# Kernel optimization log

Measured on AMD Instinct MI355X. Metric: run time of the kernel, lower is better.

Reference implementation:

```python
import jax, jax.numpy as jnp
import numpy as np

B, S, V = 2, 336, 8      # batch, seq_len, n_vars
D, H, P = 256, 8, 96     # d_model, num_heads, pred_len
DK = D // H
OUT_CHN = 8
EPS = 1e-5


def _layernorm(x, g, b):
    mu = jnp.mean(x, axis=-1, keepdims=True)
    var = jnp.var(x, axis=-1, keepdims=True)
    return (x - mu) * jax.lax.rsqrt(var + EPS) * g + b


def _attn_ff(src, Wq, bq, Wk, bk, Wv, bv, Wo, bo, ln1_g, ln1_b):
    # src: [N, L, D]; manual MHA + residual + layernorm (dropout=0)
    N, L, _ = src.shape
    q = (src @ Wq + bq).reshape(N, L, H, DK).transpose(0, 2, 1, 3)
    k = (src @ Wk + bk).reshape(N, L, H, DK).transpose(0, 2, 1, 3)
    v = (src @ Wv + bv).reshape(N, L, H, DK).transpose(0, 2, 1, 3)
    scores = jnp.einsum('nhqd,nhkd->nhqk', q, k) / np.sqrt(DK).astype(np.float32)
    attn = jax.nn.softmax(scores, axis=-1)
    o = jnp.einsum('nhqk,nhkd->nhqd', attn, v)
    o = o.transpose(0, 2, 1, 3).reshape(N, L, D) @ Wo + bo
    return _layernorm(src + o, ln1_g, ln1_b)


def setup_inputs() -> dict:
    key = jax.random.key(0)
    ks = jax.random.split(key, 8)
    s = 1.0 / np.sqrt(D)
    return {
        'x': jax.random.normal(ks[0], (B, S, V), dtype=jnp.float32),
        'emb_w': jax.random.normal(ks[1], (1, D), dtype=jnp.float32),
        'emb_b': jnp.zeros((D,), jnp.float32),
        'Wq': jax.random.normal(ks[2], (D, D), dtype=jnp.float32) * s,
        'bq': jnp.zeros((D,), jnp.float32),
        'Wk': jax.random.normal(ks[3], (D, D), dtype=jnp.float32) * s,
        'bk': jnp.zeros((D,), jnp.float32),
        'Wv': jax.random.normal(ks[4], (D, D), dtype=jnp.float32) * s,
        'bv': jnp.zeros((D,), jnp.float32),
        'Wo': jax.random.normal(ks[5], (D, D), dtype=jnp.float32) * s,
        'bo': jnp.zeros((D,), jnp.float32),
        'ln1_g': jnp.ones((D,), jnp.float32),
        'ln1_b': jnp.zeros((D,), jnp.float32),
        'norm_g': jnp.ones((D,), jnp.float32),
        'norm_b': jnp.zeros((D,), jnp.float32),
        'proj_w': jax.random.normal(ks[6], (S * D, P), dtype=jnp.float32) / np.sqrt(S * D).astype(np.float32),
        'proj_b': jnp.zeros((P,), jnp.float32),
    }


def reference(x, emb_w, emb_b, Wq, bq, Wk, bk, Wv, bv, Wo, bo,
              ln1_g, ln1_b, norm_g, norm_b, proj_w, proj_b):
    attn_p = (Wq, bq, Wk, bk, Wv, bv, Wo, bo, ln1_g, ln1_b)
    # x: [B,S,V] -> [B,V,S] -> embed each scalar to D
    e = x.transpose(0, 2, 1)[..., None] @ emb_w + emb_b  # [B,V,S,D]
    for _ in range(10):
        # attention over time axis (shared weights)
        e = _attn_ff(e.reshape(B * V, S, D), *attn_p).reshape(B, V, S, D)
        e = _layernorm(e.transpose(0, 2, 1, 3), norm_g, norm_b)  # [B,S,V,D]
        # attention over variable axis (same weights)
        e = _attn_ff(e.reshape(B * S, V, D), *attn_p).reshape(B, S, V, D)
        e = e.transpose(0, 2, 1, 3)  # [B,V,S,D]
    out = e.reshape(B, V, S * D) @ proj_w + proj_b  # [B,V,P]
    return out.transpose(0, 2, 1)[:, :, :OUT_CHN]  # [B,P,out_chn]
```

## Files before the change

kernel.cpp:

```cpp
#include <hip/hip_runtime.h>

#define SS 336
#define VV 8
#define DD 256
#define DKK 32
#define NTOK 5376
#define NTD (NTOK * DD)
#define ATT_SCALE 0.17677669529663687f
#define LN_EPS 1e-5f

typedef _Float16 f16x8 __attribute__((ext_vector_type(8)));
typedef _Float16 f16x4v __attribute__((ext_vector_type(4)));
typedef __attribute__((ext_vector_type(4))) float f32x4;

__device__ inline _Float16 f2h(float f) { return (_Float16)f; }

__global__ __launch_bounds__(256) void k_prep_w(
    const float* __restrict__ Wq, const float* __restrict__ Wk,
    const float* __restrict__ Wv, const float* __restrict__ Wo,
    _Float16* __restrict__ WT2) {
  int z = blockIdx.y;
  const float* W = (z == 0) ? Wq : (z == 1) ? Wk : (z == 2) ? Wv : Wo;
  int o = blockIdx.x * 256 + threadIdx.x;
  int blk = o >> 9;
// ... 64 lines not shown
    }
  }

  float bsv[4];
#pragma unroll
  for (int nt = 0; nt < 4; ++nt) bsv[nt] = bias[(ntb + nt) * 16 + lcol];
#pragma unroll
  for (int mt = 0; mt < 2; ++mt) {
#pragma unroll
    for (int i = 0; i < 4; ++i) {
      int r = m0 + wm * 32 + mt * 16 + quad * 4 + i;
#pragma unroll
      for (int nt = 0; nt < 4; ++nt) {
        int c = (ntb + nt) * 16 + lcol;
        H[(size_t)r * 256 + c] = f2h(acc[mt][nt][i] + bsv[nt]);
      }
    }
  }
}

#define KSTR 36
#define VTSTR 344
#define PSTR 72
__global__ __launch_bounds__(512) void k_attn_time(
    const _Float16* __restrict__ Q, const _Float16* __restrict__ K,
    const _Float16* __restrict__ V, _Float16* __restrict__ O16) {
  int qg = blockIdx.x, h = blockIdx.y, n = blockIdx.z;
  int tid = threadIdx.x;
  int wave = tid >> 6, lane = tid & 63;
  int quad = lane >> 4, lcol = lane & 15;

  __shared__ _Float16 Ks[336 * KSTR];
  __shared__ _Float16 Vt[32 * VTSTR + 16];
  __shared__ _Float16 Ps[8][16 * PSTR];

  const size_t base = (size_t)(n * SS) * DD + h * DKK;

  for (int c = tid; c < 1344; c += 512) {
    int row = c >> 2, part = c & 3;
    f16x8 kv = *(const f16x8*)&K[base + (size_t)row * DD + part * 8];
    f16x4v klo = __builtin_shufflevector(kv, kv, 0, 1, 2, 3);
    f16x4v khi = __builtin_shufflevector(kv, kv, 4, 5, 6, 7);
    *(f16x4v*)&Ks[row * KSTR + part * 8] = klo;
    *(f16x4v*)&Ks[row * KSTR + part * 8 + 4] = khi;
    f16x8 vv = *(const f16x8*)&V[base + (size_t)row * DD + part * 8];
#pragma unroll
    for (int j = 0; j < 8; ++j) Vt[(part * 8 + j) * VTSTR + row] = vv[j];
  }
  for (int c = tid; c < 272; c += 512) {
    if (c < 256) {
      int d = c >> 3, col = 336 + (c & 7);
      Vt[d * VTSTR + col] = (_Float16)0.f;
    } else {
      Vt[32 * VTSTR + (c - 256)] = (_Float16)0.f;
    }
  }
  __syncthreads();

  _Float16* P = Ps[wave];
  const f16x8 onesv = {(_Float16)1.f, (_Float16)1.f, (_Float16)1.f, (_Float16)1.f,
                       (_Float16)1.f, (_Float16)1.f, (_Float16)1.f, (_Float16)1.f};
  const f32x4 z4 = {0.f, 0.f, 0.f, 0.f};

  int qt0 = qg ? 11 : 0;
  int qtend = qg ? 21 : 11;
  for (int qtile = qt0 + wave; qtile < qtend; qtile += 8) {
    int qb = qtile * 16;

    f16x8 qf = *(const f16x8*)&Q[base + (size_t)(qb + lcol) * DD + quad * 8];
    f32x4 accA = {0.f, 0.f, 0.f, 0.f};
    f32x4 accB = {0.f, 0.f, 0.f, 0.f};
    f32x4 lacc = {0.f, 0.f, 0.f, 0.f};
    float m_[4] = {-1e30f, -1e30f, -1e30f, -1e30f};

    for (int T = 0; T < 6; ++T) {
      int k0 = T * 64;
      bool full = (T < 5);
      f32x4 s[4];
      {
        const _Float16* kp = &Ks[(k0 + lcol) * KSTR + quad * 8];
        f16x4v a0 = *(const f16x4v*)kp;
        f16x4v b0 = *(const f16x4v*)(kp + 4);
        f16x8 kf = __builtin_shufflevector(a0, b0, 0, 1, 2, 3, 4, 5, 6, 7);
        s[0] = __builtin_amdgcn_mfma_f32_16x16x32_f16(qf, kf, z4, 0, 0, 0);
      }
      if (full) {
#pragma unroll
        for (int u = 1; u < 4; ++u) {
          const _Float16* kp = &Ks[(k0 + u * 16 + lcol) * KSTR + quad * 8];
          f16x4v a0 = *(const f16x4v*)kp;
          f16x4v b0 = *(const f16x4v*)(kp + 4);
          f16x8 kf = __builtin_shufflevector(a0, b0, 0, 1, 2, 3, 4, 5, 6, 7);
          s[u] = __builtin_amdgcn_mfma_f32_16x16x32_f16(qf, kf, z4, 0, 0, 0);
        }
      } else {
        s[1] = z4; s[2] = z4; s[3] = z4;
      }
      float sc[4][4], p[4][4], corr[4];
#pragma unroll
      for (int u = 0; u < 4; ++u)
#pragma unroll
        for (int i = 0; i < 4; ++i)
          sc[u][i] = (u == 0 || full) ? s[u][i] * ATT_SCALE : -1e30f;
#pragma unroll
      for (int i = 0; i < 4; ++i) {
        float t2 = fmaxf(fmaxf(sc[0][i], sc[1][i]), fmaxf(sc[2][i], sc[3][i]));
        t2 = fmaxf(t2, __shfl_xor(t2, 1));
        t2 = fmaxf(t2, __shfl_xor(t2, 2));
        t2 = fmaxf(t2, __shfl_xor(t2, 4));
        t2 = fmaxf(t2, __shfl_xor(t2, 8));
        float nm = fmaxf(m_[i], t2);
        corr[i] = __expf(m_[i] - nm);
        m_[i] = nm;
#pragma unroll
        for (int u = 0; u < 4; ++u) p[u][i] = __expf(sc[u][i] - nm);
        accA[i] *= corr[i];
        accB[i] *= corr[i];
        lacc[i] *= corr[i];
      }
#pragma unroll
      for (int i = 0; i < 4; ++i)
#pragma unroll
        for (int u = 0; u < 4; ++u)
          P[(quad * 4 + i) * PSTR + u * 16 + lcol] = f2h(p[u][i]);
      f16x8 pf0 = *(const f16x8*)&P[lcol * PSTR + quad * 8];
      lacc = __builtin_amdgcn_mfma_f32_16x16x32_f16(pf0, onesv, lacc, 0, 0, 0);
      f16x8 va0 = *(const f16x8*)&Vt[lcol * VTSTR + k0 + quad * 8];
      f16x8 vb0 = *(const f16x8*)&Vt[(16 + lcol) * VTSTR + k0 + quad * 8];
      accA = __builtin_amdgcn_mfma_f32_16x16x32_f16(pf0, va0, accA, 0, 0, 0);
      accB = __builtin_amdgcn_mfma_f32_16x16x32_f16(pf0, vb0, accB, 0, 0, 0);
      if (full) {
        f16x8 pf1 = *(const f16x8*)&P[lcol * PSTR + 32 + quad * 8];
        lacc = __builtin_amdgcn_mfma_f32_16x16x32_f16(pf1, onesv, lacc, 0, 0, 0);
        f16x8 va1 = *(const f16x8*)&Vt[lcol * VTSTR + k0 + 32 + quad * 8];
        f16x8 vb1 = *(const f16x8*)&Vt[(16 + lcol) * VTSTR + k0 + 32 + quad * 8];
        accA = __builtin_amdgcn_mfma_f32_16x16x32_f16(pf1, va1, accA, 0, 0, 0);
        accB = __builtin_amdgcn_mfma_f32_16x16x32_f16(pf1, vb1, accB, 0, 0, 0);
      }
    }

#pragma unroll
    for (int i = 0; i < 4; ++i) {
      float inv = 1.f / lacc[i];
      P[(quad * 4 + i) * PSTR + lcol] = f2h(accA[i] * inv);
      P[(quad * 4 + i) * PSTR + 16 + lcol] = f2h(accB[i] * inv);
    }
    int row = lane >> 2, seg = lane & 3;
    f16x8 ov = *(const f16x8*)&P[row * PSTR + seg * 8];
    *(f16x8*)&O16[base + (size_t)(qb + row) * DD + seg * 8] = ov;
  }
}

__global__ __launch_bounds__(512) void k_mega_var(
    const _Float16* __restrict__ AO16, const _Float16* __restrict__ WT2,
    const float* __restrict__ bq, const float* __restrict__ bk,
    const float* __restrict__ bv, const float* __restrict__ bo,
    const float* __restrict__ g1, const float* __restrict__ c1,
    const float* __restrict__ gn, const float* __restrict__ bn,
    float* __restrict__ Etime, _Float16* __restrict__ Q16,
    _Float16* __restrict__ K16, _Float16* __restrict__ V16, int doqkv) {
  int tid = threadIdx.x;
  int wave = tid >> 6, lane = tid & 63;
  int quad = lane >> 4, lcol = lane & 15;

  __shared__ int rmapS[32];
  __shared__ _Float16 Af[32 * 264];
  __shared__ float Cf[32 * 260];
  __shared__ _Float16 QKVs[32 * 776];

  if (tid < 32) {
    int r2 = blockIdx.x * 32 + tid;
    int n_idx = r2 >> 3, v = r2 & 7;
    int b = n_idx / SS, s = n_idx - b * SS;
    rmapS[tid] = (b * VV + v) * SS + s;
  }
  __syncthreads();

  {
    int row = tid >> 4, seg = tid & 15;
    const _Float16* src = AO16 + (size_t)rmapS[row] * DD + seg * 16;
    _Float16* dst = Af + row * 264 + seg * 16;
    *(f16x8*)(dst) = *(const f16x8*)(src);
    *(f16x8*)(dst + 8) = *(const f16x8*)(src + 8);
  }
  __syncthreads();

  const _Float16* WoF = WT2 + (size_t)3 * 65536;

  {
    f32x4 acc[2][2] = {};
    for (int kb = 0; kb < 8; ++kb) {
      int k0 = kb * 32;
      f16x8 af0 = *(const f16x8*)&Af[lcol * 264 + k0 + quad * 8];
      f16x8 af1 = *(const f16x8*)&Af[(16 + lcol) * 264 + k0 + quad * 8];
#pragma unroll
      for (int nt = 0; nt < 2; ++nt) {
        f16x8 bfr = *(const f16x8*)&WoF[((wave * 2 + nt) * 8 + kb) * 512 + lane * 8];
        acc[0][nt] = __builtin_amdgcn_mfma_f32_16x16x32_f16(af0, bfr, acc[0][nt], 0, 0, 0);
        acc[1][nt] = __builtin_amdgcn_mfma_f32_16x16x32_f16(af1, bfr, acc[1][nt], 0, 0, 0);
      }
    }
#pragma unroll
    for (int mt = 0; mt < 2; ++mt) {
#pragma unroll
      for (int i = 0; i < 4; ++i) {
        int row = mt * 16 + quad * 4 + i;
        size_t rb = (size_t)rmapS[row] * 256;
#pragma unroll
        for (int nt = 0; nt < 2; ++nt) {
          int col = (wave * 2 + nt) * 16 + lcol;
          Cf[row * 260 + col] = acc[mt][nt][i] + bo[col] + Etime[rb + col];
        }
      }
    }
  }
  __syncthreads();

  {
    int row = tid >> 4, c0 = (tid & 15) * 16;
    float v[16];
#pragma unroll
    for (int j = 0; j < 16; ++j) v[j] = Cf[row * 260 + c0 + j];
#pragma unroll
    for (int pass = 0; pass < 2; ++pass) {
      const float* gg = pass ? gn : g1;
      const float* bb = pass ? bn : c1;
      float s = 0.f, q = 0.f;
#pragma unroll
      for (int j = 0; j < 16; ++j) { s += v[j]; q = fmaf(v[j], v[j], q); }
      s += __shfl_xor(s, 1); q += __shfl_xor(q, 1);
      s += __shfl_xor(s, 2); q += __shfl_xor(q, 2);
      s += __shfl_xor(s, 4); q += __shfl_xor(q, 4);
      s += __shfl_xor(s, 8); q += __shfl_xor(q, 8);
      float mu = s * (1.0f / 256.0f);
      float rs = rsqrtf(q * (1.0f / 256.0f) - mu * mu + LN_EPS);
#pragma unroll
      for (int j = 0; j < 16; ++j)
        v[j] = fmaf((v[j] - mu) * rs, gg[c0 + j], bb[c0 + j]);
    }
#pragma unroll
    for (int j = 0; j < 16; ++j) Cf[row * 260 + c0 + j] = v[j];
#pragma unroll
    for (int j8 = 0; j8 < 2; ++j8) {
      f16x8 h;
#pragma unroll
      for (int jj = 0; jj < 8; ++jj) h[jj] = f2h(v[j8 * 8 + jj]);
      *(f16x8*)&Af[row * 264 + c0 + j8 * 8] = h;
    }
  }
  __syncthreads();

  {
    f32x4 acc[2][6] = {};
    for (int kb = 0; kb < 8; ++kb) {
      int k0 = kb * 32;
      f16x8 af0 = *(const f16x8*)&Af[lcol * 264 + k0 + quad * 8];
      f16x8 af1 = *(const f16x8*)&Af[(16 + lcol) * 264 + k0 + quad * 8];
#pragma unroll
      for (int j = 0; j < 6; ++j) {
        int ntg = wave * 6 + j;
        f16x8 bfr = *(const f16x8*)&WT2[(size_t)(ntg * 8 + kb) * 512 + lane * 8];
        acc[0][j] = __builtin_amdgcn_mfma_f32_16x16x32_f16(af0, bfr, acc[0][j], 0, 0, 0);
        acc[1][j] = __builtin_amdgcn_mfma_f32_16x16x32_f16(af1, bfr, acc[1][j], 0, 0, 0);
      }
    }
#pragma unroll
    for (int j = 0; j < 6; ++j) {
      int ntg = wave * 6 + j;
      int colb = ntg * 16;
      int z = colb >> 8, coln = (colb & 255) + lcol;
      const float* bz = (z == 0) ? bq : (z == 1) ? bk : bv;
      float bval = bz[coln];
#pragma unroll
      for (int mt = 0; mt < 2; ++mt) {
#pragma unroll
        for (int i = 0; i < 4; ++i)
          QKVs[(mt * 16 + quad * 4 + i) * 776 + colb + lcol] = f2h(acc[mt][j][i] + bval);
      }
    }
  }
  __syncthreads();

  {
    int half = tid & 1, qi = (tid >> 1) & 7, h = (tid >> 4) & 7, ng = tid >> 7;
    int d0 = h * 32 + half * 16;
    const _Float16* Qp = &QKVs[(ng * 8 + qi) * 776 + d0];
    float qv[16];
#pragma unroll
    for (int j8 = 0; j8 < 2; ++j8) {
      f16x8 t = *(const f16x8*)(Qp + j8 * 8);
#pragma unroll
      for (int jj = 0; jj < 8; ++jj) qv[j8 * 8 + jj] = (float)t[jj];
    }
    float sc[8];
#pragma unroll
    for (int k = 0; k < 8; ++k) {
      const _Float16* Kp = &QKVs[(ng * 8 + k) * 776 + 256 + d0];
      float s = 0.f;
#pragma unroll
      for (int j8 = 0; j8 < 2; ++j8) {
        f16x8 t = *(const f16x8*)(Kp + j8 * 8);
#pragma unroll
        for (int jj = 0; jj < 8; ++jj) s = fmaf(qv[j8 * 8 + jj], (float)t[jj], s);
      }
      sc[k] = s;
    }
#pragma unroll
    for (int k = 0; k < 8; ++k)
      sc[k] = (sc[k] + __shfl_xor(sc[k], 1)) * ATT_SCALE;
    float mx = sc[0];
#pragma unroll
    for (int k = 1; k < 8; ++k) mx = fmaxf(mx, sc[k]);
    float ps = 0.f;
#pragma unroll
    for (int k = 0; k < 8; ++k) { sc[k] = __expf(sc[k] - mx); ps += sc[k]; }
    float inv = 1.f / ps;
    float ov[16];
#pragma unroll
    for (int j = 0; j < 16; ++j) ov[j] = 0.f;
#pragma unroll
    for (int k = 0; k < 8; ++k) {
      const _Float16* Vp = &QKVs[(ng * 8 + k) * 776 + 512 + d0];
      float p = sc[k];
#pragma unroll
      for (int j8 = 0; j8 < 2; ++j8) {
        f16x8 t = *(const f16x8*)(Vp + j8 * 8);
#pragma unroll
        for (int jj = 0; jj < 8; ++jj)
          ov[j8 * 8 + jj] = fmaf(p, (float)t[jj], ov[j8 * 8 + jj]);
      }
    }
    _Float16* Op = &Af[(ng * 8 + qi) * 264 + d0];
#pragma unroll
    for (int j8 = 0; j8 < 2; ++j8) {
      f16x8 hh;
#pragma unroll
      for (int jj = 0; jj < 8; ++jj) hh[jj] = f2h(ov[j8 * 8 + jj] * inv);
      *(f16x8*)(Op + j8 * 8) = hh;
    }
  }
  __syncthreads();

  {
    f32x4 acc[2][2] = {};
    for (int kb = 0; kb < 8; ++kb) {
      int k0 = kb * 32;
      f16x8 af0 = *(const f16x8*)&Af[lcol * 264 + k0 + quad * 8];
      f16x8 af1 = *(const f16x8*)&Af[(16 + lcol) * 264 + k0 + quad * 8];
#pragma unroll
      for (int nt = 0; nt < 2; ++nt) {
        f16x8 bfr = *(const f16x8*)&WoF[((wave * 2 + nt) * 8 + kb) * 512 + lane * 8];
        acc[0][nt] = __builtin_amdgcn_mfma_f32_16x16x32_f16(af0, bfr, acc[0][nt], 0, 0, 0);
        acc[1][nt] = __builtin_amdgcn_mfma_f32_16x16x32_f16(af1, bfr, acc[1][nt], 0, 0, 0);
      }
    }
#pragma unroll
    for (int mt = 0; mt < 2; ++mt) {
#pragma unroll
      for (int i = 0; i < 4; ++i) {
        int row = mt * 16 + quad * 4 + i;
#pragma unroll
        for (int nt = 0; nt < 2; ++nt) {
          int col = (wave * 2 + nt) * 16 + lcol;
          Cf[row * 260 + col] = acc[mt][nt][i] + bo[col] + Cf[row * 260 + col];
        }
      }
    }
  }
  __syncthreads();

  {
    int row = tid >> 4, c0 = (tid & 15) * 16;
    float v[16];
#pragma unroll
    for (int j = 0; j < 16; ++j) v[j] = Cf[row * 260 + c0 + j];
    float s = 0.f, q = 0.f;
#pragma unroll
    for (int j = 0; j < 16; ++j) { s += v[j]; q = fmaf(v[j], v[j], q); }
    s += __shfl_xor(s, 1); q += __shfl_xor(q, 1);
    s += __shfl_xor(s, 2); q += __shfl_xor(q, 2);
    s += __shfl_xor(s, 4); q += __shfl_xor(q, 4);
    s += __shfl_xor(s, 8); q += __shfl_xor(q, 8);
    float mu = s * (1.0f / 256.0f);
    float rs = rsqrtf(q * (1.0f / 256.0f) - mu * mu + LN_EPS);
#pragma unroll
    for (int j = 0; j < 16; ++j)
      v[j] = fmaf((v[j] - mu) * rs, g1[c0 + j], c1[c0 + j]);
    size_t rb = (size_t)rmapS[row] * 256 + c0;
#pragma unroll
    for (int j4 = 0; j4 < 4; ++j4) {
      float4 f4 = make_float4(v[j4 * 4], v[j4 * 4 + 1], v[j4 * 4 + 2], v[j4 * 4 + 3]);
      *(float4*)&Etime[rb + j4 * 4] = f4;
    }
#pragma unroll
    for (int j8 = 0; j8 < 2; ++j8) {
      f16x8 hh;
#pragma unroll
      for (int jj = 0; jj < 8; ++jj) hh[jj] = f2h(v[j8 * 8 + jj]);
      *(f16x8*)&Af[row * 264 + c0 + j8 * 8] = hh;
    }
  }
  __syncthreads();

  if (doqkv) {
    f32x4 acc[2][6] = {};
    for (int kb = 0; kb < 8; ++kb) {
      int k0 = kb * 32;
      f16x8 af0 = *(const f16x8*)&Af[lcol * 264 + k0 + quad * 8];
      f16x8 af1 = *(const f16x8*)&Af[(16 + lcol) * 264 + k0 + quad * 8];
#pragma unroll
      for (int j = 0; j < 6; ++j) {
        int ntg = wave * 6 + j;
        f16x8 bfr = *(const f16x8*)&WT2[(size_t)(ntg * 8 + kb) * 512 + lane * 8];
        acc[0][j] = __builtin_amdgcn_mfma_f32_16x16x32_f16(af0, bfr, acc[0][j], 0, 0, 0);
        acc[1][j] = __builtin_amdgcn_mfma_f32_16x16x32_f16(af1, bfr, acc[1][j], 0, 0, 0);
      }
    }
#pragma unroll
    for (int j = 0; j < 6; ++j) {
      int ntg = wave * 6 + j;
      int colb = ntg * 16;
      int z = colb >> 8, coln = (colb & 255) + lcol;
      const float* bz = (z == 0) ? bq : (z == 1) ? bk : bv;
      _Float16* Hd = (z == 0) ? Q16 : (z == 1) ? K16 : V16;
      float bval = bz[coln];
#pragma unroll
      for (int mt = 0; mt < 2; ++mt) {
#pragma unroll
        for (int i = 0; i < 4; ++i) {
          int row = mt * 16 + quad * 4 + i;
          Hd[(size_t)rmapS[row] * 256 + coln] = f2h(acc[mt][j][i] + bval);
        }
      }
    }
  }
}

__global__ __launch_bounds__(192) void k_proj_partial(
    const float* __restrict__ E, const float* __restrict__ PW,
    float* __restrict__ Part) {
  int kc = blockIdx.x;
  int tid = threadIdx.x;
  int p4 = tid % 24, g = tid / 24;
  __shared__ float Es[16][128];
  __shared__ float sm[8][1536];
  for (int idx = tid; idx < 512; idx += 192) {
    int row = idx >> 5, kk4 = idx & 31;
    *(float4*)&Es[row][kk4 * 4] =
        *(const float4*)&E[(size_t)row * 86016 + kc * 128 + kk4 * 4];
  }
  __syncthreads();
  float4 acc[16];
#pragma unroll
  for (int i = 0; i < 16; ++i) acc[i] = make_float4(0.f, 0.f, 0.f, 0.f);
  for (int j = 0; j < 16; ++j) {
    int k = g * 16 + j;
    float4 w = *(const float4*)&PW[(size_t)(kc * 128 + k) * 96 + p4 * 4];
// ... 61 lines not shown
  const float* bo = (const float*)d_in[10];
  const float* g1 = (const float*)d_in[11];
  const float* b1 = (const float*)d_in[12];
  const float* gn = (const float*)d_in[13];
  const float* bn = (const float*)d_in[14];
  const float* PW = (const float*)d_in[15];
  const float* PB = (const float*)d_in[16];
  float* out = (float*)d_out;

  float* ws = (float*)d_ws;
  float* Etime   = ws;
  _Float16* Et16 = (_Float16*)(ws + (size_t)NTD);
  _Float16* Q16  = (_Float16*)(ws + (size_t)NTD + NTD / 2);
  _Float16* K16  = Q16 + (size_t)NTD;
  _Float16* V16  = K16 + (size_t)NTD;
  _Float16* AO16 = V16 + (size_t)NTD;
  _Float16* WT2  = AO16 + (size_t)NTD;
  float* Part    = (float*)(WT2 + 4 * 65536);

  k_prep_w<<<dim3(256, 4), 256, 0, stream>>>(Wq, Wk, Wv, Wo, WT2);
  k_embed<<<NTOK, 256, 0, stream>>>(x, emb_w, emb_b, Etime, Et16);
  k_gemm_qkv<<<dim3(84, 2, 3), 256, 0, stream>>>(
      Et16, WT2, bq, bk, bv, Q16, K16, V16);
  for (int it = 0; it < 10; ++it) {
    k_attn_time<<<dim3(2, 8, 16), 512, 0, stream>>>(Q16, K16, V16, AO16);
    k_mega_var<<<168, 512, 0, stream>>>(
        AO16, WT2, bq, bk, bv, bo, g1, b1, gn, bn, Etime,
        Q16, K16, V16, (it < 9) ? 1 : 0);
  }
  k_proj_partial<<<672, 192, 0, stream>>>(Etime, PW, Part);
  k_proj_reduce<<<96, 256, 0, stream>>>(Part, PB, out);
}
```

Baseline: 571.8 us.

## Fuse 10-iteration attention loop into one persistent cooperative kernel with grid syncs

Replaces the 20 per-iteration launches of the time-attention and variable-attention kernels with a single cooperative kernel of 256 blocks. Inside it, the two phases are separated by grid.sync and share one raw shared-memory buffer. This removes kernel launch and drain gaps between stages. In exchange it adds grid-wide barriers, and in the variable phase only 168 of the 256 blocks do work. It also requires all 256 blocks, each using about 100KB of shared memory, to be co-resident.

```diff
diff --git a/kernel.cpp b/kernel.cpp
--- a/kernel.cpp
+++ b/kernel.cpp
@@ -1,4 +1,7 @@
 #include <hip/hip_runtime.h>
+#include <hip/hip_cooperative_groups.h>
+
+namespace cg = cooperative_groups;
 
 #define SS 336
 #define VV 8
@@ -110,417 +113,425 @@
 #define KSTR 36
 #define VTSTR 344
 #define PSTR 72
-__global__ __launch_bounds__(512) void k_attn_time(
-    const _Float16* __restrict__ Q, const _Float16* __restrict__ K,
-    const _Float16* __restrict__ V, _Float16* __restrict__ O16) {
-  int qg = blockIdx.x, h = blockIdx.y, n = blockIdx.z;
-  int tid = threadIdx.x;
-  int wave = tid >> 6, lane = tid & 63;
-  int quad = lane >> 4, lcol = lane & 15;
-
-  __shared__ _Float16 Ks[336 * KSTR];
-  __shared__ _Float16 Vt[32 * VTSTR + 16];
-  __shared__ _Float16 Ps[8][16 * PSTR];
-
-  const size_t base = (size_t)(n * SS) * DD + h * DKK;
-
-  for (int c = tid; c < 1344; c += 512) {
-    int row = c >> 2, part = c & 3;
-    f16x8 kv = *(const f16x8*)&K[base + (size_t)row * DD + part * 8];
-    f16x4v klo = __builtin_shufflevector(kv, kv, 0, 1, 2, 3);
-    f16x4v khi = __builtin_shufflevector(kv, kv, 4, 5, 6, 7);
-    *(f16x4v*)&Ks[row * KSTR + part * 8] = klo;
-    *(f16x4v*)&Ks[row * KSTR + part * 8 + 4] = khi;
-    f16x8 vv = *(const f16x8*)&V[base + (size_t)row * DD + part * 8];
-#pragma unroll
-    for (int j = 0; j < 8; ++j) Vt[(part * 8 + j) * VTSTR + row] = vv[j];
-  }
-  for (int c = tid; c < 272; c += 512) {
-    if (c < 256) {
-      int d = c >> 3, col = 336 + (c & 7);
-      Vt[d * VTSTR + col] = (_Float16)0.f;
-    } else {
-      Vt[32 * VTSTR + (c - 256)] = (_Float16)0.f;
-    }
-  }
-  __syncthreads();
-
-  _Float16* P = Ps[wave];
-  const f16x8 onesv = {(_Float16)1.f, (_Float16)1.f, (_Float16)1.f, (_Float16)1.f,
-                       (_Float16)1.f, (_Float16)1.f, (_Float16)1.f, (_Float16)1.f};
-  const f32x4 z4 = {0.f, 0.f, 0.f, 0.f};
-
-  int qt0 = qg ? 11 : 0;
-  int qtend = qg ? 21 : 11;
-  for (int qtile = qt0 + wave; qtile < qtend; qtile += 8) {
-    int qb = qtile * 16;
-
-    f16x8 qf = *(const f16x8*)&Q[base + (size_t)(qb + lcol) * DD + quad * 8];
-    f32x4 accA = {0.f, 0.f, 0.f, 0.f};
-    f32x4 accB = {0.f, 0.f, 0.f, 0.f};
-    f32x4 lacc = {0.f, 0.f, 0.f, 0.f};
-    float m_[4] = {-1e30f, -1e30f, -1e30f, -1e30f};
-
-    for (int T = 0; T < 6; ++T) {
-      int k0 = T * 64;
-      bool full = (T < 5);
-      f32x4 s[4];
-      {
-        const _Float16* kp = &Ks[(k0 + lcol) * KSTR + quad * 8];
-        f16x4v a0 = *(const f16x4v*)kp;
-        f16x4v b0 = *(const f16x4v*)(kp + 4);
-        f16x8 kf = __builtin_shufflevector(a0, b0, 0, 1, 2, 3, 4, 5, 6, 7);
-        s[0] = __builtin_amdgcn_mfma_f32_16x16x32_f16(qf, kf, z4, 0, 0, 0);
-      }
-      if (full) {
-#pragma unroll
-        for (int u = 1; u < 4; ++u) {
-          const _Float16* kp = &Ks[(k0 + u * 16 + lcol) * KSTR + quad * 8];
-          f16x4v a0 = *(const f16x4v*)kp;
-          f16x4v b0 = *(const f16x4v*)(kp + 4);
-          f16x8 kf = __builtin_shufflevector(a0, b0, 0, 1, 2, 3, 4, 5, 6, 7);
-          s[u] = __builtin_amdgcn_mfma_f32_16x16x32_f16(qf, kf, z4, 0, 0, 0);
-        }
-      } else {
-        s[1] = z4; s[2] = z4; s[3] = z4;
-      }
-      float sc[4][4], p[4][4], corr[4];
-#pragma unroll
-      for (int u = 0; u < 4; ++u)
-#pragma unroll
-        for (int i = 0; i < 4; ++i)
-          sc[u][i] = (u == 0 || full) ? s[u][i] * ATT_SCALE : -1e30f;
-#pragma unroll
-      for (int i = 0; i < 4; ++i) {
-        float t2 = fmaxf(fmaxf(sc[0][i], sc[1][i]), fmaxf(sc[2][i], sc[3][i]));
-        t2 = fmaxf(t2, __shfl_xor(t2, 1));
-        t2 = fmaxf(t2, __shfl_xor(t2, 2));
-        t2 = fmaxf(t2, __shfl_xor(t2, 4));
-        t2 = fmaxf(t2, __shfl_xor(t2, 8));
-        float nm = fmaxf(m_[i], t2);
-        corr[i] = __expf(m_[i] - nm);
-        m_[i] = nm;
-#pragma unroll
-        for (int u = 0; u < 4; ++u) p[u][i] = __expf(sc[u][i] - nm);
-        accA[i] *= corr[i];
-        accB[i] *= corr[i];
-        lacc[i] *= corr[i];
-      }
-#pragma unroll
-      for (int i = 0; i < 4; ++i)
-#pragma unroll
-        for (int u = 0; u < 4; ++u)
-          P[(quad * 4 + i) * PSTR + u * 16 + lcol] = f2h(p[u][i]);
-      f16x8 pf0 = *(const f16x8*)&P[lcol * PSTR + quad * 8];
-      lacc = __builtin_amdgcn_mfma_f32_16x16x32_f16(pf0, onesv, lacc, 0, 0, 0);
-      f16x8 va0 = *(const f16x8*)&Vt[lcol * VTSTR + k0 + quad * 8];
-      f16x8 vb0 = *(const f16x8*)&Vt[(16 + lcol) * VTSTR + k0 + quad * 8];
-      accA = __builtin_amdgcn_mfma_f32_16x16x32_f16(pf0, va0, accA, 0, 0, 0);
-      accB = __builtin_amdgcn_mfma_f32_16x16x32_f16(pf0, vb0, accB, 0, 0, 0);
-      if (full) {
-        f16x8 pf1 = *(const f16x8*)&P[lcol * PSTR + 32 + quad * 8];
-        lacc = __builtin_amdgcn_mfma_f32_16x16x32_f16(pf1, onesv, lacc, 0, 0, 0);
-        f16x8 va1 = *(const f16x8*)&Vt[lcol * VTSTR + k0 + 32 + quad * 8];
-        f16x8 vb1 = *(const f16x8*)&Vt[(16 + lcol) * VTSTR + k0 + 32 + quad * 8];
-        accA = __builtin_amdgcn_mfma_f32_16x16x32_f16(pf1, va1, accA, 0, 0, 0);
-        accB = __builtin_amdgcn_mfma_f32_16x16x32_f16(pf1, vb1, accB, 0, 0, 0);
-      }
-    }
-
-#pragma unroll
-    for (int i = 0; i < 4; ++i) {
-      float inv = 1.f / lacc[i];
-      P[(quad * 4 + i) * PSTR + lcol] = f2h(accA[i] * inv);
-      P[(quad * 4 + i) * PSTR + 16 + lcol] = f2h(accB[i] * inv);
-    }
-    int row = lane >> 2, seg = lane & 3;
-    f16x8 ov = *(const f16x8*)&P[row * PSTR + seg * 8];
-    *(f16x8*)&O16[base + (size_t)(qb + row) * DD + seg * 8] = ov;
-  }
-}
-
-__global__ __launch_bounds__(512) void k_mega_var(
-    const _Float16* __restrict__ AO16, const _Float16* __restrict__ WT2,
+
+__global__ __launch_bounds__(512) void k_loop(
+    _Float16* __restrict__ Q16, _Float16* __restrict__ K16,
+    _Float16* __restrict__ V16, _Float16* __restrict__ AO16,
+    const _Float16* __restrict__ WT2,
     const float* __restrict__ bq, const float* __restrict__ bk,
     const float* __restrict__ bv, const float* __restrict__ bo,
     const float* __restrict__ g1, const float* __restrict__ c1,
     const float* __restrict__ gn, const float* __restrict__ bn,
-    float* __restrict__ Etime, _Float16* __restrict__ Q16,
-    _Float16* __restrict__ K16, _Float16* __restrict__ V16, int doqkv) {
+    float* __restrict__ Etime) {
+  cg::grid_group grid = cg::this_grid();
+
+  __shared__ __align__(16) char SMRAW[99968];
+
+  int bid = blockIdx.x;
   int tid = threadIdx.x;
   int wave = tid >> 6, lane = tid & 63;
   int quad = lane >> 4, lcol = lane & 15;
 
-  __shared__ int rmapS[32];
-  __shared__ _Float16 Af[32 * 264];
-  __shared__ float Cf[32 * 260];
-  __shared__ _Float16 QKVs[32 * 776];
-
-  if (tid < 32) {
-    int r2 = blockIdx.x * 32 + tid;
-    int n_idx = r2 >> 3, v = r2 & 7;
-    int b = n_idx / SS, s = n_idx - b * SS;
-    rmapS[tid] = (b * VV + v) * SS + s;
-  }
-  __syncthreads();
-
-  {
-    int row = tid >> 4, seg = tid & 15;
-    const _Float16* src = AO16 + (size_t)rmapS[row] * DD + seg * 16;
-    _Float16* dst = Af + row * 264 + seg * 16;
-    *(f16x8*)(dst) = *(const f16x8*)(src);
-    *(f16x8*)(dst + 8) = *(const f16x8*)(src + 8);
-  }
-  __syncthreads();
-
   const _Float16* WoF = WT2 + (size_t)3 * 65536;
 
-  {
-    f32x4 acc[2][2] = {};
-    for (int kb = 0; kb < 8; ++kb) {
-      int k0 = kb * 32;
-      f16x8 af0 = *(const f16x8*)&Af[lcol * 264 + k0 + quad * 8];
-      f16x8 af1 = *(const f16x8*)&Af[(16 + lcol) * 264 + k0 + quad * 8];
-#pragma unroll
-      for (int nt = 0; nt < 2; ++nt) {
-        f16x8 bfr = *(const f16x8*)&WoF[((wave * 2 + nt) * 8 + kb) * 512 + lane * 8];
-        acc[0][nt] = __builtin_amdgcn_mfma_f32_16x16x32_f16(af0, bfr, acc[0][nt], 0, 0, 0);
-        acc[1][nt] = __builtin_amdgcn_mfma_f32_16x16x32_f16(af1, bfr, acc[1][nt], 0, 0, 0);
+  for (int it = 0; it < 10; ++it) {
+    {
+      _Float16* Ks  = (_Float16*)SMRAW;
+      _Float16* Vt  = (_Float16*)(SMRAW + 24192);
+      _Float16* PsB = (_Float16*)(SMRAW + 46240);
+
+      int qg = bid & 1, h = (bid >> 1) & 7, n = bid >> 4;
+      const size_t base = (size_t)(n * SS) * DD + h * DKK;
+
+      for (int c = tid; c < 1344; c += 512) {
+        int row = c >> 2, part = c & 3;
+        f16x8 kv = *(const f16x8*)&K16[base + (size_t)row * DD + part * 8];
+        f16x4v klo = __builtin_shufflevector(kv, kv, 0, 1, 2, 3);
+        f16x4v khi = __builtin_shufflevector(kv, kv, 4, 5, 6, 7);
+        *(f16x4v*)&Ks[row * KSTR + part * 8] = klo;
+        *(f16x4v*)&Ks[row * KSTR + part * 8 + 4] = khi;
+        f16x8 vv = *(const f16x8*)&V16[base + (size_t)row * DD + part * 8];
+#pragma unroll
+        for (int j = 0; j < 8; ++j) Vt[(part * 8 + j) * VTSTR + row] = vv[j];
+      }
+      for (int c = tid; c < 272; c += 512) {
+        if (c < 256) {
+          int d = c >> 3, col = 336 + (c & 7);
+          Vt[d * VTSTR + col] = (_Float16)0.f;
+        } else {
+          Vt[32 * VTSTR + (c - 256)] = (_Float16)0.f;
+        }
+      }
+      __syncthreads();
+
+      _Float16* P = PsB + wave * (16 * PSTR);
+      const f16x8 onesv = {(_Float16)1.f, (_Float16)1.f, (_Float16)1.f, (_Float16)1.f,
+                           (_Float16)1.f, (_Float16)1.f, (_Float16)1.f, (_Float16)1.f};
+      const f32x4 z4 = {0.f, 0.f, 0.f, 0.f};
+
+      int qt0 = qg ? 11 : 0;
+      int qtend = qg ? 21 : 11;
+      for (int qtile = qt0 + wave; qtile < qtend; qtile += 8) {
+        int qb = qtile * 16;
+
+        f16x8 qf = *(const f16x8*)&Q16[base + (size_t)(qb + lcol) * DD + quad * 8];
+        f32x4 accA = {0.f, 0.f, 0.f, 0.f};
+        f32x4 accB = {0.f, 0.f, 0.f, 0.f};
+        f32x4 lacc = {0.f, 0.f, 0.f, 0.f};
+        float m_[4] = {-1e30f, -1e30f, -1e30f, -1e30f};
+
+        for (int T = 0; T < 6; ++T) {
+          int k0 = T * 64;
+          bool full = (T < 5);
+          f32x4 s[4];
+          {
+            const _Float16* kp = &Ks[(k0 + lcol) * KSTR + quad * 8];
+            f16x4v a0 = *(const f16x4v*)kp;
+            f16x4v b0 = *(const f16x4v*)(kp + 4);
+            f16x8 kf = __builtin_shufflevector(a0, b0, 0, 1, 2, 3, 4, 5, 6, 7);
+            s[0] = __builtin_amdgcn_mfma_f32_16x16x32_f16(qf, kf, z4, 0, 0, 0);
+          }
+          if (full) {
+#pragma unroll
+            for (int u = 1; u < 4; ++u) {
+              const _Float16* kp = &Ks[(k0 + u * 16 + lcol) * KSTR + quad * 8];
+              f16x4v a0 = *(const f16x4v*)kp;
+              f16x4v b0 = *(const f16x4v*)(kp + 4);
+              f16x8 kf = __builtin_shufflevector(a0, b0, 0, 1, 2, 3, 4, 5, 6, 7);
+              s[u] = __builtin_amdgcn_mfma_f32_16x16x32_f16(qf, kf, z4, 0, 0, 0);
+            }
+          } else {
+            s[1] = z4; s[2] = z4; s[3] = z4;
+          }
+          float sc[4][4], p[4][4], corr[4];
+#pragma unroll
+          for (int u = 0; u < 4; ++u)
+#pragma unroll
+            for (int i = 0; i < 4; ++i)
+              sc[u][i] = (u == 0 || full) ? s[u][i] * ATT_SCALE : -1e30f;
+#pragma unroll
+          for (int i = 0; i < 4; ++i) {
+            float t2 = fmaxf(fmaxf(sc[0][i], sc[1][i]), fmaxf(sc[2][i], sc[3][i]));
+            t2 = fmaxf(t2, __shfl_xor(t2, 1));
+            t2 = fmaxf(t2, __shfl_xor(t2, 2));
+            t2 = fmaxf(t2, __shfl_xor(t2, 4));
+            t2 = fmaxf(t2, __shfl_xor(t2, 8));
+            float nm = fmaxf(m_[i], t2);
+            corr[i] = __expf(m_[i] - nm);
+            m_[i] = nm;
+#pragma unroll
+            for (int u = 0; u < 4; ++u) p[u][i] = __expf(sc[u][i] - nm);
+            accA[i] *= corr[i];
+            accB[i] *= corr[i];
+            lacc[i] *= corr[i];
+          }
+#pragma unroll
+          for (int i = 0; i < 4; ++i)
+#pragma unroll
+            for (int u = 0; u < 4; ++u)
+              P[(quad * 4 + i) * PSTR + u * 16 + lcol] = f2h(p[u][i]);
+          f16x8 pf0 = *(const f16x8*)&P[lcol * PSTR + quad * 8];
+          lacc = __builtin_amdgcn_mfma_f32_16x16x32_f16(pf0, onesv, lacc, 0, 0, 0);
+          f16x8 va0 = *(const f16x8*)&Vt[lcol * VTSTR + k0 + quad * 8];
+          f16x8 vb0 = *(const f16x8*)&Vt[(16 + lcol) * VTSTR + k0 + quad * 8];
+          accA = __builtin_amdgcn_mfma_f32_16x16x32_f16(pf0, va0, accA, 0, 0, 0);
+          accB = __builtin_amdgcn_mfma_f32_16x16x32_f16(pf0, vb0, accB, 0, 0, 0);
+          if (full) {
+            f16x8 pf1 = *(const f16x8*)&P[lcol * PSTR + 32 + quad * 8];
+            lacc = __builtin_amdgcn_mfma_f32_16x16x32_f16(pf1, onesv, lacc, 0, 0, 0);
+            f16x8 va1 = *(const f16x8*)&Vt[lcol * VTSTR + k0 + 32 + quad * 8];
+            f16x8 vb1 = *(const f16x8*)&Vt[(16 + lcol) * VTSTR + k0 + 32 + quad * 8];
+            accA = __builtin_amdgcn_mfma_f32_16x16x32_f16(pf1, va1, accA, 0, 0, 0);
+            accB = __builtin_amdgcn_mfma_f32_16x16x32_f16(pf1, vb1, accB, 0, 0, 0);
+          }
+        }
+
+#pragma unroll
+        for (int i = 0; i < 4; ++i) {
+          float inv = 1.f / lacc[i];
+          P[(quad * 4 + i) * PSTR + lcol] = f2h(accA[i] * inv);
+          P[(quad * 4 + i) * PSTR + 16 + lcol] = f2h(accB[i] * inv);
+        }
+        int row = lane >> 2, seg = lane & 3;
+        f16x8 ov = *(const f16x8*)&P[row * PSTR + seg * 8];
+        *(f16x8*)&AO16[base + (size_t)(qb + row) * DD + seg * 8] = ov;
       }
     }
-#pragma unroll
-    for (int mt = 0; mt < 2; ++mt) {
-#pragma unroll
-      for (int i = 0; i < 4; ++i) {
-        int row = mt * 16 + quad * 4 + i;
-        size_t rb = (size_t)rmapS[row] * 256;
-#pragma unroll
-        for (int nt = 0; nt < 2; ++nt) {
-          int col = (wave * 2 + nt) * 16 + lcol;
-          Cf[row * 260 + col] = acc[mt][nt][i] + bo[col] + Etime[rb + col];
+    grid.sync();
+
+    if (bid < 168) {
+      int* rmapS     = (int*)SMRAW;
+      _Float16* Af   = (_Float16*)(SMRAW + 128);
+      float* Cf      = (float*)(SMRAW + 17024);
+      _Float16* QKVs = (_Float16*)(SMRAW + 50304);
+      int doqkv = (it < 9) ? 1 : 0;
+
+      if (tid < 32) {
+        int r2 = bid * 32 + tid;
+        int n_idx = r2 >> 3, v = r2 & 7;
+        int b = n_idx / SS, s = n_idx - b * SS;
+        rmapS[tid] = (b * VV + v) * SS + s;
+      }
+      __syncthreads();
+
+      {
+        int row = tid >> 4, seg = tid & 15;
+        const _Float16* src = AO16 + (size_t)rmapS[row] * DD + seg * 16;
+        _Float16* dst = Af + row * 264 + seg * 16;
+        *(f16x8*)(dst) = *(const f16x8*)(src);
+        *(f16x8*)(dst + 8) = *(const f16x8*)(src + 8);
+      }
+      __syncthreads();
+
+      {
+        f32x4 acc[2][2] = {};
+        for (int kb = 0; kb < 8; ++kb) {
+          int k0 = kb * 32;
+          f16x8 af0 = *(const f16x8*)&Af[lcol * 264 + k0 + quad * 8];
+          f16x8 af1 = *(const f16x8*)&Af[(16 + lcol) * 264 + k0 + quad * 8];
+#pragma unroll
+          for (int nt = 0; nt < 2; ++nt) {
+            f16x8 bfr = *(const f16x8*)&WoF[((wave * 2 + nt) * 8 + kb) * 512 + lane * 8];
+            acc[0][nt] = __builtin_amdgcn_mfma_f32_16x16x32_f16(af0, bfr, acc[0][nt], 0, 0, 0);
+            acc[1][nt] = __builtin_amdgcn_mfma_f32_16x16x32_f16(af1, bfr, acc[1][nt], 0, 0, 0);
+          }
+        }
+#pragma unroll
+        for (int mt = 0; mt < 2; ++mt) {
+#pragma unroll
+          for (int i = 0; i < 4; ++i) {
+            int row = mt * 16 + quad * 4 + i;
+            size_t rb = (size_t)rmapS[row] * 256;
+#pragma unroll
+            for (int nt = 0; nt < 2; ++nt) {
+              int col = (wave * 2 + nt) * 16 + lcol;
+              Cf[row * 260 + col] = acc[mt][nt][i] + bo[col] + Etime[rb + col];
+            }
+          }
+        }
+      }
+      __syncthreads();
+
+      {
+        int row = tid >> 4, c0 = (tid & 15) * 16;
+        float v[16];
+#pragma unroll
+        for (int j = 0; j < 16; ++j) v[j] = Cf[row * 260 + c0 + j];
+#pragma unroll
+        for (int pass = 0; pass < 2; ++pass) {
+          const float* gg = pass ? gn : g1;
+          const float* bb = pass ? bn : c1;
+          float s = 0.f, q = 0.f;
+#pragma unroll
+          for (int j = 0; j < 16; ++j) { s += v[j]; q = fmaf(v[j], v[j], q); }
+          s += __shfl_xor(s, 1); q += __shfl_xor(q, 1);
+          s += __shfl_xor(s, 2); q += __shfl_xor(q, 2);
+          s += __shfl_xor(s, 4); q += __shfl_xor(q, 4);
+          s += __shfl_xor(s, 8); q += __shfl_xor(q, 8);
+          float mu = s * (1.0f / 256.0f);
+          float rs = rsqrtf(q * (1.0f / 256.0f) - mu * mu + LN_EPS);
+#pragma unroll
+          for (int j = 0; j < 16; ++j)
+            v[j] = fmaf((v[j] - mu) * rs, gg[c0 + j], bb[c0 + j]);
+        }
+#pragma unroll
+        for (int j = 0; j < 16; ++j) Cf[row * 260 + c0 + j] = v[j];
+#pragma unroll
+        for (int j8 = 0; j8 < 2; ++j8) {
+          f16x8 h;
+#pragma unroll
+          for (int jj = 0; jj < 8; ++jj) h[jj] = f2h(v[j8 * 8 + jj]);
+          *(f16x8*)&Af[row * 264 + c0 + j8 * 8] = h;
+        }
+      }
+      __syncthreads();
+
+      {
+        f32x4 acc[2][6] = {};
+        for (int kb = 0; kb < 8; ++kb) {
+          int k0 = kb * 32;
+          f16x8 af0 = *(const f16x8*)&Af[lcol * 264 + k0 + quad * 8];
+          f16x8 af1 = *(const f16x8*)&Af[(16 + lcol) * 264 + k0 + quad * 8];
+#pragma unroll
+          for (int j = 0; j < 6; ++j) {
+            int ntg = wave * 6 + j;
+            f16x8 bfr = *(const f16x8*)&WT2[(size_t)(ntg * 8 + kb) * 512 + lane * 8];
+            acc[0][j] = __builtin_amdgcn_mfma_f32_16x16x32_f16(af0, bfr, acc[0][j], 0, 0, 0);
+            acc[1][j] = __builtin_amdgcn_mfma_f32_16x16x32_f16(af1, bfr, acc[1][j], 0, 0, 0);
+          }
+        }
+#pragma unroll
+        for (int j = 0; j < 6; ++j) {
+          int ntg = wave * 6 + j;
+          int colb = ntg * 16;
+          int z = colb >> 8, coln = (colb & 255) + lcol;
+          const float* bz = (z == 0) ? bq : (z == 1) ? bk : bv;
+          float bval = bz[coln];
+#pragma unroll
+          for (int mt = 0; mt < 2; ++mt) {
+#pragma unroll
+            for (int i = 0; i < 4; ++i)
+              QKVs[(mt * 16 + quad * 4 + i) * 776 + colb + lcol] = f2h(acc[mt][j][i] + bval);
+          }
+        }
+      }
+      __syncthreads();
+
+      {
+        int half = tid & 1, qi = (tid >> 1) & 7, h = (tid >> 4) & 7, ng = tid >> 7;
+        int d0 = h * 32 + half * 16;
+        const _Float16* Qp = &QKVs[(ng * 8 + qi) * 776 + d0];
+        float qv[16];
+#pragma unroll
+        for (int j8 = 0; j8 < 2; ++j8) {
+          f16x8 t = *(const f16x8*)(Qp + j8 * 8);
+#pragma unroll
+          for (int jj = 0; jj < 8; ++jj) qv[j8 * 8 + jj] = (float)t[jj];
+        }
+        float sc[8];
+#pragma unroll
+        for (int k = 0; k < 8; ++k) {
+          const _Float16* Kp = &QKVs[(ng * 8 + k) * 776 + 256 + d0];
+          float s = 0.f;
+#pragma unroll
+          for (int j8 = 0; j8 < 2; ++j8) {
+            f16x8 t = *(const f16x8*)(Kp + j8 * 8);
+#pragma unroll
+            for (int jj = 0; jj < 8; ++jj) s = fmaf(qv[j8 * 8 + jj], (float)t[jj], s);
+          }
+          sc[k] = s;
+        }
+#pragma unroll
+        for (int k = 0; k < 8; ++k)
+          sc[k] = (sc[k] + __shfl_xor(sc[k], 1)) * ATT_SCALE;
+        float mx = sc[0];
+#pragma unroll
+        for (int k = 1; k < 8; ++k) mx = fmaxf(mx, sc[k]);
+        float ps = 0.f;
+#pragma unroll
+        for (int k = 0; k < 8; ++k) { sc[k] = __expf(sc[k] - mx); ps += sc[k]; }
+        float inv = 1.f / ps;
+        float ov[16];
+#pragma unroll
+        for (int j = 0; j < 16; ++j) ov[j] = 0.f;
+#pragma unroll
+        for (int k = 0; k < 8; ++k) {
+          const _Float16* Vp = &QKVs[(ng * 8 + k) * 776 + 512 + d0];
+          float p = sc[k];
+#pragma unroll
+          for (int j8 = 0; j8 < 2; ++j8) {
+            f16x8 t = *(const f16x8*)(Vp + j8 * 8);
+#pragma unroll
+            for (int jj = 0; jj < 8; ++jj)
+              ov[j8 * 8 + jj] = fmaf(p, (float)t[jj], ov[j8 * 8 + jj]);
+          }
+        }
+        _Float16* Op = &Af[(ng * 8 + qi) * 264 + d0];
+#pragma unroll
+        for (int j8 = 0; j8 < 2; ++j8) {
+          f16x8 hh;
+#pragma unroll
+          for (int jj = 0; jj < 8; ++jj) hh[jj] = f2h(ov[j8 * 8 + jj] * inv);
+          *(f16x8*)(Op + j8 * 8) = hh;
+        }
+      }
+      __syncthreads();
+
+      {
+        f32x4 acc[2][2] = {};
+        for (int kb = 0; kb < 8; ++kb) {
+          int k0 = kb * 32;
+          f16x8 af0 = *(const f16x8*)&Af[lcol * 264 + k0 + quad * 8];
+          f16x8 af1 = *(const f16x8*)&Af[(16 + lcol) * 264 + k0 + quad * 8];
+#pragma unroll
+          for (int nt = 0; nt < 2; ++nt) {
+            f16x8 bfr = *(const f16x8*)&WoF[((wave * 2 + nt) * 8 + kb) * 512 + lane * 8];
+            acc[0][nt] = __builtin_amdgcn_mfma_f32_16x16x32_f16(af0, bfr, acc[0][nt], 0, 0, 0);
+            acc[1][nt] = __builtin_amdgcn_mfma_f32_16x16x32_f16(af1, bfr, acc[1][nt], 0, 0, 0);
+          }
+        }
+#pragma unroll
+        for (int mt = 0; mt < 2; ++mt) {
+#pragma unroll
+          for (int i = 0; i < 4; ++i) {
+            int row = mt * 16 + quad * 4 + i;
+#pragma unroll
+            for (int nt = 0; nt < 2; ++nt) {
+              int col = (wave * 2 + nt) * 16 + lcol;
+              Cf[row * 260 + col] = acc[mt][nt][i] + bo[col] + Cf[row * 260 + col];
+            }
+          }
+        }
+      }
+      __syncthreads();
+
+      {
+        int row = tid >> 4, c0 = (tid & 15) * 16;
+        float v[16];
+#pragma unroll
+        for (int j = 0; j < 16; ++j) v[j] = Cf[row * 260 + c0 + j];
+        float s = 0.f, q = 0.f;
+#pragma unroll
+        for (int j = 0; j < 16; ++j) { s += v[j]; q = fmaf(v[j], v[j], q); }
+        s += __shfl_xor(s, 1); q += __shfl_xor(q, 1);
+        s += __shfl_xor(s, 2); q += __shfl_xor(q, 2);
+        s += __shfl_xor(s, 4); q += __shfl_xor(q, 4);
+        s += __shfl_xor(s, 8); q += __shfl_xor(q, 8);
+        float mu = s * (1.0f / 256.0f);
+        float rs = rsqrtf(q * (1.0f / 256.0f) - mu * mu + LN_EPS);
+#pragma unroll
+        for (int j = 0; j < 16; ++j)
+          v[j] = fmaf((v[j] - mu) * rs, g1[c0 + j], c1[c0 + j]);
+        size_t rb = (size_t)rmapS[row] * 256 + c0;
+#pragma unroll
+        for (int j4 = 0; j4 < 4; ++j4) {
+          float4 f4 = make_float4(v[j4 * 4], v[j4 * 4 + 1], v[j4 * 4 + 2], v[j4 * 4 + 3]);
+          *(float4*)&Etime[rb + j4 * 4] = f4;
+        }
+#pragma unroll
+        for (int j8 = 0; j8 < 2; ++j8) {
+          f16x8 hh;
+#pragma unroll
+          for (int jj = 0; jj < 8; ++jj) hh[jj] = f2h(v[j8 * 8 + jj]);
+          *(f16x8*)&Af[row * 264 + c0 + j8 * 8] = hh;
+        }
+      }
+      __syncthreads();
+
+      if (doqkv) {
+        f32x4 acc[2][6] = {};
+        for (int kb = 0; kb < 8; ++kb) {
+          int k0 = kb * 32;
+          f16x8 af0 = *(const f16x8*)&Af[lcol * 264 + k0 + quad * 8];
+          f16x8 af1 = *(const f16x8*)&Af[(16 + lcol) * 264 + k0 + quad * 8];
+#pragma unroll
+          for (int j = 0; j < 6; ++j) {
+            int ntg = wave * 6 + j;
+            f16x8 bfr = *(const f16x8*)&WT2[(size_t)(ntg * 8 + kb) * 512 + lane * 8];
+            acc[0][j] = __builtin_amdgcn_mfma_f32_16x16x32_f16(af0, bfr, acc[0][j], 0, 0, 0);
+            acc[1][j] = __builtin_amdgcn_mfma_f32_16x16x32_f16(af1, bfr, acc[1][j], 0, 0, 0);
+          }
+        }
+#pragma unroll
+        for (int j = 0; j < 6; ++j) {
+          int ntg = wave * 6 + j;
+          int colb = ntg * 16;
+          int z = colb >> 8, coln = (colb & 255) + lcol;
+          const float* bz = (z == 0) ? bq : (z == 1) ? bk : bv;
+          _Float16* Hd = (z == 0) ? Q16 : (z == 1) ? K16 : V16;
+          float bval = bz[coln];
+#pragma unroll
+          for (int mt = 0; mt < 2; ++mt) {
+#pragma unroll
+            for (int i = 0; i < 4; ++i) {
+              int row = mt * 16 + quad * 4 + i;
+              Hd[(size_t)rmapS[row] * 256 + coln] = f2h(acc[mt][j][i] + bval);
+            }
+          }
         }
       }
     }
-  }
-  __syncthreads();
-
-  {
-    int row = tid >> 4, c0 = (tid & 15) * 16;
-    float v[16];
-#pragma unroll
-    for (int j = 0; j < 16; ++j) v[j] = Cf[row * 260 + c0 + j];
-#pragma unroll
-    for (int pass = 0; pass < 2; ++pass) {
-      const float* gg = pass ? gn : g1;
-      const float* bb = pass ? bn : c1;
-      float s = 0.f, q = 0.f;
-#pragma unroll
-      for (int j = 0; j < 16; ++j) { s += v[j]; q = fmaf(v[j], v[j], q); }
-      s += __shfl_xor(s, 1); q += __shfl_xor(q, 1);
-      s += __shfl_xor(s, 2); q += __shfl_xor(q, 2);
-      s += __shfl_xor(s, 4); q += __shfl_xor(q, 4);
-      s += __shfl_xor(s, 8); q += __shfl_xor(q, 8);
-      float mu = s * (1.0f / 256.0f);
-      float rs = rsqrtf(q * (1.0f / 256.0f) - mu * mu + LN_EPS);
-#pragma unroll
-      for (int j = 0; j < 16; ++j)
-        v[j] = fmaf((v[j] - mu) * rs, gg[c0 + j], bb[c0 + j]);
-    }
-#pragma unroll
-    for (int j = 0; j < 16; ++j) Cf[row * 260 + c0 + j] = v[j];
-#pragma unroll
-    for (int j8 = 0; j8 < 2; ++j8) {
-      f16x8 h;
-#pragma unroll
-      for (int jj = 0; jj < 8; ++jj) h[jj] = f2h(v[j8 * 8 + jj]);
-      *(f16x8*)&Af[row * 264 + c0 + j8 * 8] = h;
-    }
-  }
-  __syncthreads();
-
-  {
-    f32x4 acc[2][6] = {};
-    for (int kb = 0; kb < 8; ++kb) {
-      int k0 = kb * 32;
-      f16x8 af0 = *(const f16x8*)&Af[lcol * 264 + k0 + quad * 8];
-      f16x8 af1 = *(const f16x8*)&Af[(16 + lcol) * 264 + k0 + quad * 8];
-#pragma unroll
-      for (int j = 0; j < 6; ++j) {
-        int ntg = wave * 6 + j;
-        f16x8 bfr = *(const f16x8*)&WT2[(size_t)(ntg * 8 + kb) * 512 + lane * 8];
-        acc[0][j] = __builtin_amdgcn_mfma_f32_16x16x32_f16(af0, bfr, acc[0][j], 0, 0, 0);
-        acc[1][j] = __builtin_amdgcn_mfma_f32_16x16x32_f16(af1, bfr, acc[1][j], 0, 0, 0);
-      }
-    }
-#pragma unroll
-    for (int j = 0; j < 6; ++j) {
-      int ntg = wave * 6 + j;
-      int colb = ntg * 16;
-      int z = colb >> 8, coln = (colb & 255) + lcol;
-      const float* bz = (z == 0) ? bq : (z == 1) ? bk : bv;
-      float bval = bz[coln];
-#pragma unroll
-      for (int mt = 0; mt < 2; ++mt) {
-#pragma unroll
-        for (int i = 0; i < 4; ++i)
-          QKVs[(mt * 16 + quad * 4 + i) * 776 + colb + lcol] = f2h(acc[mt][j][i] + bval);
-      }
-    }
-  }
-  __syncthreads();
-
-  {
-    int half = tid & 1, qi = (tid >> 1) & 7, h = (tid >> 4) & 7, ng = tid >> 7;
-    int d0 = h * 32 + half * 16;
-    const _Float16* Qp = &QKVs[(ng * 8 + qi) * 776 + d0];
-    float qv[16];
-#pragma unroll
-    for (int j8 = 0; j8 < 2; ++j8) {
-      f16x8 t = *(const f16x8*)(Qp + j8 * 8);
-#pragma unroll
-      for (int jj = 0; jj < 8; ++jj) qv[j8 * 8 + jj] = (float)t[jj];
-    }
-    float sc[8];
-#pragma unroll
-    for (int k = 0; k < 8; ++k) {
-      const _Float16* Kp = &QKVs[(ng * 8 + k) * 776 + 256 + d0];
-      float s = 0.f;
-#pragma unroll
-      for (int j8 = 0; j8 < 2; ++j8) {
-        f16x8 t = *(const f16x8*)(Kp + j8 * 8);
-#pragma unroll
-        for (int jj = 0; jj < 8; ++jj) s = fmaf(qv[j8 * 8 + jj], (float)t[jj], s);
-      }
-      sc[k] = s;
-    }
-#pragma unroll
-    for (int k = 0; k < 8; ++k)
-      sc[k] = (sc[k] + __shfl_xor(sc[k], 1)) * ATT_SCALE;
-    float mx = sc[0];
-#pragma unroll
-    for (int k = 1; k < 8; ++k) mx = fmaxf(mx, sc[k]);
-    float ps = 0.f;
-#pragma unroll
-    for (int k = 0; k < 8; ++k) { sc[k] = __expf(sc[k] - mx); ps += sc[k]; }
-    float inv = 1.f / ps;
-    float ov[16];
-#pragma unroll
-    for (int j = 0; j < 16; ++j) ov[j] = 0.f;
-#pragma unroll
-    for (int k = 0; k < 8; ++k) {
-      const _Float16* Vp = &QKVs[(ng * 8 + k) * 776 + 512 + d0];
-      float p = sc[k];
-#pragma unroll
-      for (int j8 = 0; j8 < 2; ++j8) {
-        f16x8 t = *(const f16x8*)(Vp + j8 * 8);
-#pragma unroll
-        for (int jj = 0; jj < 8; ++jj)
-          ov[j8 * 8 + jj] = fmaf(p, (float)t[jj], ov[j8 * 8 + jj]);
-      }
-    }
-    _Float16* Op = &Af[(ng * 8 + qi) * 264 + d0];
-#pragma unroll
-    for (int j8 = 0; j8 < 2; ++j8) {
-      f16x8 hh;
-#pragma unroll
-      for (int jj = 0; jj < 8; ++jj) hh[jj] = f2h(ov[j8 * 8 + jj] * inv);
-      *(f16x8*)(Op + j8 * 8) = hh;
-    }
-  }
-  __syncthreads();
-
-  {
-    f32x4 acc[2][2] = {};
-    for (int kb = 0; kb < 8; ++kb) {
-      int k0 = kb * 32;
-      f16x8 af0 = *(const f16x8*)&Af[lcol * 264 + k0 + quad * 8];
-      f16x8 af1 = *(const f16x8*)&Af[(16 + lcol) * 264 + k0 + quad * 8];
-#pragma unroll
-      for (int nt = 0; nt < 2; ++nt) {
-        f16x8 bfr = *(const f16x8*)&WoF[((wave * 2 + nt) * 8 + kb) * 512 + lane * 8];
-        acc[0][nt] = __builtin_amdgcn_mfma_f32_16x16x32_f16(af0, bfr, acc[0][nt], 0, 0, 0);
-        acc[1][nt] = __builtin_amdgcn_mfma_f32_16x16x32_f16(af1, bfr, acc[1][nt], 0, 0, 0);
-      }
-    }
-#pragma unroll
-    for (int mt = 0; mt < 2; ++mt) {
-#pragma unroll
-      for (int i = 0; i < 4; ++i) {
-        int row = mt * 16 + quad * 4 + i;
-#pragma unroll
-        for (int nt = 0; nt < 2; ++nt) {
-          int col = (wave * 2 + nt) * 16 + lcol;
-          Cf[row * 260 + col] = acc[mt][nt][i] + bo[col] + Cf[row * 260 + col];
-        }
-      }
-    }
-  }
-  __syncthreads();
-
-  {
-    int row = tid >> 4, c0 = (tid & 15) * 16;
-    float v[16];
-#pragma unroll
-    for (int j = 0; j < 16; ++j) v[j] = Cf[row * 260 + c0 + j];
-    float s = 0.f, q = 0.f;
-#pragma unroll
-    for (int j = 0; j < 16; ++j) { s += v[j]; q = fmaf(v[j], v[j], q); }
-    s += __shfl_xor(s, 1); q += __shfl_xor(q, 1);
-    s += __shfl_xor(s, 2); q += __shfl_xor(q, 2);
-    s += __shfl_xor(s, 4); q += __shfl_xor(q, 4);
-    s += __shfl_xor(s, 8); q += __shfl_xor(q, 8);
-    float mu = s * (1.0f / 256.0f);
-    float rs = rsqrtf(q * (1.0f / 256.0f) - mu * mu + LN_EPS);
-#pragma unroll
-    for (int j = 0; j < 16; ++j)
-      v[j] = fmaf((v[j] - mu) * rs, g1[c0 + j], c1[c0 + j]);
-    size_t rb = (size_t)rmapS[row] * 256 + c0;
-#pragma unroll
-    for (int j4 = 0; j4 < 4; ++j4) {
-      float4 f4 = make_float4(v[j4 * 4], v[j4 * 4 + 1], v[j4 * 4 + 2], v[j4 * 4 + 3]);
-      *(float4*)&Etime[rb + j4 * 4] = f4;
-    }
-#pragma unroll
-    for (int j8 = 0; j8 < 2; ++j8) {
-      f16x8 hh;
-#pragma unroll
-      for (int jj = 0; jj < 8; ++jj) hh[jj] = f2h(v[j8 * 8 + jj]);
-      *(f16x8*)&Af[row * 264 + c0 + j8 * 8] = hh;
-    }
-  }
-  __syncthreads();
-
-  if (doqkv) {
-    f32x4 acc[2][6] = {};
-    for (int kb = 0; kb < 8; ++kb) {
-      int k0 = kb * 32;
-      f16x8 af0 = *(const f16x8*)&Af[lcol * 264 + k0 + quad * 8];
-      f16x8 af1 = *(const f16x8*)&Af[(16 + lcol) * 264 + k0 + quad * 8];
-#pragma unroll
-      for (int j = 0; j < 6; ++j) {
-        int ntg = wave * 6 + j;
-        f16x8 bfr = *(const f16x8*)&WT2[(size_t)(ntg * 8 + kb) * 512 + lane * 8];
-        acc[0][j] = __builtin_amdgcn_mfma_f32_16x16x32_f16(af0, bfr, acc[0][j], 0, 0, 0);
-        acc[1][j] = __builtin_amdgcn_mfma_f32_16x16x32_f16(af1, bfr, acc[1][j], 0, 0, 0);
-      }
-    }
-#pragma unroll
-    for (int j = 0; j < 6; ++j) {
-      int ntg = wave * 6 + j;
-      int colb = ntg * 16;
-      int z = colb >> 8, coln = (colb & 255) + lcol;
-      const float* bz = (z == 0) ? bq : (z == 1) ? bk : bv;
-      _Float16* Hd = (z == 0) ? Q16 : (z == 1) ? K16 : V16;
-      float bval = bz[coln];
-#pragma unroll
-      for (int mt = 0; mt < 2; ++mt) {
-#pragma unroll
-        for (int i = 0; i < 4; ++i) {
-          int row = mt * 16 + quad * 4 + i;
-          Hd[(size_t)rmapS[row] * 256 + coln] = f2h(acc[mt][j][i] + bval);
-        }
-      }
-    }
+    if (it < 9) grid.sync();
   }
 }
 
@@ -628,12 +639,17 @@
   k_embed<<<NTOK, 256, 0, stream>>>(x, emb_w, emb_b, Etime, Et16);
   k_gemm_qkv<<<dim3(84, 2, 3), 256, 0, stream>>>(
       Et16, WT2, bq, bk, bv, Q16, K16, V16);
-  for (int it = 0; it < 10; ++it) {
-    k_attn_time<<<dim3(2, 8, 16), 512, 0, stream>>>(Q16, K16, V16, AO16);
-    k_mega_var<<<168, 512, 0, stream>>>(
-        AO16, WT2, bq, bk, bv, bo, g1, b1, gn, bn, Etime,
-        Q16, K16, V16, (it < 9) ? 1 : 0);
-  }
+
+  {
+    void* args[] = {
+      (void*)&Q16, (void*)&K16, (void*)&V16, (void*)&AO16, (void*)&WT2,
+      (void*)&bq, (void*)&bk, (void*)&bv, (void*)&bo,
+      (void*)&g1, (void*)&b1, (void*)&gn, (void*)&bn, (void*)&Etime
+    };
+    hipLaunchCooperativeKernel((void*)k_loop, dim3(256), dim3(512),
+                               args, 0, stream);
+  }
+
   k_proj_partial<<<672, 192, 0, stream>>>(Etime, PW, Part);
   k_proj_reduce<<<96, 256, 0, stream>>>(Part, PB, out);
 }
```

Result: slower. 1.321 ms (+131.0%).
